# Optimization experiments

Measured on AMD Instinct MI355X. Metric: run time of the kernel, lower is better.

The kernel has to match this reference:

```python
import jax, jax.numpy as jnp
import numpy as np

S = 64            # out_size
EXPAND = 1.25
FEAT_DOWN = 8
DEG2RAD = np.pi / 180.0


def setup_inputs() -> dict:
    key = jax.random.key(0)
    k1, k2, k3 = jax.random.split(key, 3)
    B, C, Hf, Wf = 2, 64, 128, 128
    N = 256
    feat = jax.random.normal(k1, (B, C, Hf, Wf), dtype=jnp.float32)
    r = jax.random.uniform(k2, (N, 5), dtype=jnp.float32)
    # values chosen so the (buggy-but-faithful) normalized-coordinate affine
    # actually samples inside the feature map (see shape_source note)
    cx = (r[:, 0] - 0.5) * 10.0
    cy = (r[:, 1] - 0.5) * 10.0
    w = 50.0 + 350.0 * r[:, 2]
    h = 50.0 + 350.0 * r[:, 3]
    deg = (r[:, 4] - 0.5) * 180.0
    obb = jnp.stack([cx, cy, w, h, deg], axis=1)
    bix = jax.random.randint(k3, (N,), 0, B)
    return {"feat": feat, "obb": obb, "bix": bix}


def _grids(obb):
    """Replicates obb_to_affine + F.affine_grid(align_corners=False).
    Returns normalized grid coords gx, gy of shape (N, S, S)."""
    scale = 1.0 / FEAT_DOWN
    cx = obb[:, 0] * scale
    cy = obb[:, 1] * scale
    ws = obb[:, 2] * scale * EXPAND
    hs = obb[:, 3] * scale * EXPAND
    th = obb[:, 4] * DEG2RAD
    c = jnp.cos(th)
    s_ = jnp.sin(th)
    sx = ws / S
    sy = hs / S
    # faithful to source: M = [[c*sx, -sin*sy, cx], [expand*sx, c*sy, cy]]
    m00 = c * sx
    m01 = -s_ * sy
    m02 = cx
    m10 = EXPAND * sx   # source uses `s` = expand here, NOT sin(theta)
    m11 = c * sy
    m12 = cy
    # affine_grid base coords (align_corners=False): (2k+1)/S - 1
    base = (2.0 * jnp.arange(S, dtype=obb.dtype) + 1.0) / S - 1.0
    x = base[None, None, :]   # output column -> x
    y = base[None, :, None]   # output row    -> y
    gx = m00[:, None, None] * x + m01[:, None, None] * y + m02[:, None, None]
    gy = m10[:, None, None] * x + m11[:, None, None] * y + m12[:, None, None]
    return gx, gy


def _rotated_roi_pool(feat, obb, bix):
    B, C, Hf, Wf = feat.shape
    gx, gy = _grids(obb)                       # (N,S,S)
    # grid_sample unnormalize (align_corners=False)
    ix = ((gx + 1.0) * Wf - 1.0) * 0.5
    iy = ((gy + 1.0) * Hf - 1.0) * 0.5
    x0f = jnp.floor(ix)
    y0f = jnp.floor(iy)
    wx1 = ix - x0f
    wy1 = iy - y0f
    x0 = x0f.astype(jnp.int32)
    y0 = y0f.astype(jnp.int32)
    b = bix[:, None, None].astype(jnp.int32)   # (N,1,1)

    def corner(yi, xi):
        valid = (xi >= 0) & (xi < Wf) & (yi >= 0) & (yi < Hf)
        yc = jnp.clip(yi, 0, Hf - 1)
        xc = jnp.clip(xi, 0, Wf - 1)
        v = feat[b, :, yc, xc]                 # (N,S,S,C) gather
        return v * valid[..., None].astype(feat.dtype)

    out = (corner(y0, x0)         * ((1.0 - wy1) * (1.0 - wx1))[..., None]
         + corner(y0, x0 + 1)     * ((1.0 - wy1) * wx1)[..., None]
         + corner(y0 + 1, x0)     * (wy1 * (1.0 - wx1))[..., None]
         + corner(y0 + 1, x0 + 1) * (wy1 * wx1)[..., None])
    return jnp.transpose(out, (0, 3, 1, 2))    # (N,C,S,S)


def reference(feat, obb, bix):
    return _rotated_roi_pool(feat, obb, bix)
```

## Files before the change

kernel.cpp:

```cpp
#include <hip/hip_runtime.h>
#include <math.h>

#define S 64
#define NC 64
#define HF 128
#define WF 128
#define HW (HF * WF)
#define SS (S * S)
#define EXPANDF 1.25f
#define FEAT_DOWN_INV 0.125f
#define DEG2RADF 0.017453292519943295f

typedef float vfloat4 __attribute__((ext_vector_type(4)));

__device__ __forceinline__ unsigned int f32_to_bf16_rne(float v) {
    unsigned int u = __float_as_uint(v);
    return (u + 0x7FFFu + ((u >> 16) & 1u)) >> 16;
}
__device__ __forceinline__ float bf16_bits_to_f32(unsigned int h) {
    return __uint_as_float(h << 16);
}

__global__ __launch_bounds__(256) void nchw_to_nhwc_bf16_kernel(
    const float*    __restrict__ feat,
    unsigned short* __restrict__ featT)
{
    __shared__ float lds[64 * 65];
    const int bh  = blockIdx.x;
    const int b   = bh >> 7;
    const int h   = bh & (HF - 1);
    const int w0  = blockIdx.y << 6;
    const int tid = threadIdx.x;
    const int t4  = tid >> 6;
    const int t64 = tid & 63;

#pragma unroll
    for (int k = 0; k < 16; ++k) {
        const int c = (k << 2) + t4;
        lds[t64 * 65 + c] = feat[(((size_t)b * NC + c) * HF + h) * WF + w0 + t64];
    }
    __syncthreads();
#pragma unroll
    for (int k = 0; k < 16; ++k) {
        const int w = (k << 2) + t4;
        featT[(((size_t)b * HF + h) * WF + w0 + w) * NC + t64] =
            (unsigned short)f32_to_bf16_rne(lds[w * 65 + t64]);
    }
}

__global__ __launch_bounds__(256) void RotatedROIPool_kernel(
    const unsigned short* __restrict__ featT,
    const float*          __restrict__ obb,
    const int*            __restrict__ bix,
    float*                __restrict__ out,
    int nwg_per_xcd)
{
    __shared__ float lds[64 * 65];

    const int bid = blockIdx.x;
    const int wg  = (bid & 7) * nwg_per_xcd + (bid >> 3);
    const int n   = wg >> 6;
    const int i   = wg & 63;

    const int tid  = threadIdx.x;
    const int wv   = tid >> 6;
    const int lane = tid & 63;
    const int s    = lane >> 3;
    const int c8   = lane & 7;

    const float o0 = obb[n * 5 + 0];
    const float o1 = obb[n * 5 + 1];
    const float o2 = obb[n * 5 + 2];
    const float o3 = obb[n * 5 + 3];
    const float o4 = obb[n * 5 + 4];

    const float cx  = o0 * FEAT_DOWN_INV;
    const float cy  = o1 * FEAT_DOWN_INV;
    const float wsc = o2 * FEAT_DOWN_INV * EXPANDF;
    const float hsc = o3 * FEAT_DOWN_INV * EXPANDF;
    const float th  = o4 * DEG2RADF;

    float sth, cth;
    sincosf(th, &sth, &cth);

    const float sx  = wsc * (1.0f / (float)S);
    const float sy  = hsc * (1.0f / (float)S);
    const float m00 = cth * sx;
    const float m01 = -sth * sy;
    const float m10 = EXPANDF * sx;
    const float m11 = cth * sy;

    const float yg = (2.0f * (float)i + 1.0f) * (1.0f / (float)S) - 1.0f;
    const float hx = m01 * yg + cx;
    const float hy = m11 * yg + cy;

    const int b = bix[n];
    const unsigned char* __restrict__ pb =
        (const unsigned char*)featT + (size_t)b * ((size_t)HW * NC * 2);

#pragma unroll
    for (int sg = 0; sg < 2; ++sg) {
        const int j = (wv << 4) + (sg << 3) + s;

        const float xg = (2.0f * (float)j + 1.0f) * (1.0f / (float)S) - 1.0f;
        const float gx = m00 * xg + hx;
        const float gy = m10 * xg + hy;

        const float ix = ((gx + 1.0f) * (float)WF - 1.0f) * 0.5f;
        const float iy = ((gy + 1.0f) * (float)HF - 1.0f) * 0.5f;

        const float x0f = floorf(ix);
        const float y0f = floorf(iy);
        const float wx1 = ix - x0f;
        const float wy1 = iy - y0f;
        const float wx0 = 1.0f - wx1;
        const float wy0 = 1.0f - wy1;

        const int x0 = (int)x0f;
        const int y0 = (int)y0f;
        const int x1 = x0 + 1;
        const int y1 = y0 + 1;

        const float vx0 = (x0 >= 0 && x0 < WF) ? 1.0f : 0.0f;
        const float vx1 = (x1 >= 0 && x1 < WF) ? 1.0f : 0.0f;
        const float vy0 = (y0 >= 0 && y0 < HF) ? 1.0f : 0.0f;
        const float vy1 = (y1 >= 0 && y1 < HF) ? 1.0f : 0.0f;

        const float w00 = wy0 * wx0 * vy0 * vx0;
        const float w01 = wy0 * wx1 * vy0 * vx1;
        const float w10 = wy1 * wx0 * vy1 * vx0;
        const float w11 = wy1 * wx1 * vy1 * vx1;

        const int x0c = min(max(x0, 0), WF - 1);
        const int x1c = min(max(x1, 0), WF - 1);
        const int y0c = min(max(y0, 0), HF - 1);
        const int y1c = min(max(y1, 0), HF - 1);

        const uint4 a00 = *((const uint4*)(pb + ((size_t)(y0c * WF + x0c) << 7)) + c8);
        const uint4 a01 = *((const uint4*)(pb + ((size_t)(y0c * WF + x1c) << 7)) + c8);
        const uint4 a10 = *((const uint4*)(pb + ((size_t)(y1c * WF + x0c) << 7)) + c8);
        const uint4 a11 = *((const uint4*)(pb + ((size_t)(y1c * WF + x1c) << 7)) + c8);

        const unsigned int* u00 = (const unsigned int*)&a00;
        const unsigned int* u01 = (const unsigned int*)&a01;
        const unsigned int* u10 = (const unsigned int*)&a10;
        const unsigned int* u11 = (const unsigned int*)&a11;

        float* L = lds + j * 65 + (c8 << 3);
#pragma unroll
        for (int m = 0; m < 4; ++m) {
            const float f00l = bf16_bits_to_f32(u00[m] & 0xFFFFu);
            const float f01l = bf16_bits_to_f32(u01[m] & 0xFFFFu);
            const float f10l = bf16_bits_to_f32(u10[m] & 0xFFFFu);
            const float f11l = bf16_bits_to_f32(u11[m] & 0xFFFFu);
            const float f00h = bf16_bits_to_f32(u00[m] >> 16);
            const float f01h = bf16_bits_to_f32(u01[m] >> 16);
            const float f10h = bf16_bits_to_f32(u10[m] >> 16);
            const float f11h = bf16_bits_to_f32(u11[m] >> 16);
            L[2 * m + 0] = w00 * f00l + w01 * f01l + w10 * f10l + w11 * f11l;
            L[2 * m + 1] = w00 * f00h + w01 * f01h + w10 * f10h + w11 * f11h;
        }
    }

    __syncthreads();

    float* __restrict__ ob = out + (size_t)n * NC * SS + (size_t)i * S;
    const int jg = tid & 15;
    const int cl = tid >> 4;
#pragma unroll
    for (int k = 0; k < 4; ++k) {
        const int c = (k << 4) + cl;
        vfloat4 t;
        t.x = lds[(jg * 4 + 0) * 65 + c];
        t.y = lds[(jg * 4 + 1) * 65 + c];
        t.z = lds[(jg * 4 + 2) * 65 + c];
        t.w = lds[(jg * 4 + 3) * 65 + c];
        __builtin_nontemporal_store(t, (vfloat4*)(ob + (size_t)c * SS + (jg << 2)));
    }
}

__global__ __launch_bounds__(256) void RotatedROIPool_nchw_kernel(
    const float* __restrict__ feat, const float* __restrict__ obb,
    const int* __restrict__ bix, float* __restrict__ out)
{
    const int tid = threadIdx.x, pid = blockIdx.x;
    const int n = pid >> 4, patch = pid & 15;
    const int pi = (patch >> 2) << 4, pj = (patch & 3) << 4;
    const int w = tid >> 6, lane = tid & 63;
    const int i = pi + ((w >> 1) << 3) + (lane >> 3);
    const int j = pj + ((w & 1) << 3) + (lane & 7);
    const int c0 = blockIdx.y * 8;

    const float cx = obb[n*5+0]*FEAT_DOWN_INV, cy = obb[n*5+1]*FEAT_DOWN_INV;
    const float wsc = obb[n*5+2]*FEAT_DOWN_INV*EXPANDF, hsc = obb[n*5+3]*FEAT_DOWN_INV*EXPANDF;
    float sth, cth; sincosf(obb[n*5+4]*DEG2RADF, &sth, &cth);
    const float sx = wsc/(float)S, sy = hsc/(float)S;
    const float m00 = cth*sx, m01 = -sth*sy, m10 = EXPANDF*sx, m11 = cth*sy;
    const float xg = (2.f*j+1.f)/(float)S - 1.f, yg = (2.f*i+1.f)/(float)S - 1.f;
    const float gx = m00*xg + m01*yg + cx, gy = m10*xg + m11*yg + cy;
    const float ix = ((gx+1.f)*WF-1.f)*.5f, iy = ((gy+1.f)*HF-1.f)*.5f;
    const float x0f = floorf(ix), y0f = floorf(iy);
    const float wx1 = ix-x0f, wy1 = iy-y0f, wx0 = 1.f-wx1, wy0 = 1.f-wy1;
    const int x0 = (int)x0f, y0 = (int)y0f, x1 = x0+1, y1 = y0+1;
    const float vx0 = (x0>=0&&x0<WF)?1.f:0.f, vx1 = (x1>=0&&x1<WF)?1.f:0.f;
    const float vy0 = (y0>=0&&y0<HF)?1.f:0.f, vy1 = (y1>=0&&y1<HF)?1.f:0.f;
    const float w00 = wy0*wx0*vy0*vx0, w01 = wy0*wx1*vy0*vx1;
    const float w10 = wy1*wx0*vy1*vx0, w11 = wy1*wx1*vy1*vx1;
    const int x0c = min(max(x0,0),WF-1), x1c = min(max(x1,0),WF-1);
    const int y0c = min(max(y0,0),HF-1), y1c = min(max(y1,0),HF-1);
    const int o00 = y0c*WF+x0c, o01 = y0c*WF+x1c, o10 = y1c*WF+x0c, o11 = y1c*WF+x1c;
    const float* p = feat + (size_t)bix[n]*NC*HW + (size_t)c0*HW;
    float* op = out + (size_t)n*NC*SS + (size_t)c0*SS + (size_t)i*S + j;
#pragma unroll
    for (int g = 0; g < 2; ++g) {
        float v00[4], v01[4], v10[4], v11[4];
        const float* pc = p + (size_t)g*4*HW;
#pragma unroll
        for (int c = 0; c < 4; ++c) { v00[c]=pc[o00]; v01[c]=pc[o01]; v10[c]=pc[o10]; v11[c]=pc[o11]; pc += HW; }
        float* oc = op + (size_t)g*4*SS;
#pragma unroll
        for (int c = 0; c < 4; ++c) { *oc = w00*v00[c]+w01*v01[c]+w10*v10[c]+w11*v11[c]; oc += SS; }
    }
}

extern "C" void kernel_launch(void* const* d_in, const int* in_sizes, int n_in,
                              void* d_out, int out_size, void* d_ws, size_t ws_size,
                              hipStream_t stream) {
    const float* feat = (const float*)d_in[0];
    const float* obb  = (const float*)d_in[1];
    const int*   bx   = (const int*)d_in[2];
    float* out = (float*)d_out;

    const int N = in_sizes[1] / 5;
    const int B = in_sizes[0] / (NC * HW);
    const size_t tbytes = (size_t)B * NC * HW * sizeof(unsigned short);

    if (ws_size >= tbytes) {
        unsigned short* featT = (unsigned short*)d_ws;
        dim3 tg(B * HF, WF / 64, 1);
        nchw_to_nhwc_bf16_kernel<<<tg, 256, 0, stream>>>(feat, featT);

        const int nwg = N * S;
        RotatedROIPool_kernel<<<nwg, 256, 0, stream>>>(featT, obb, bx, out, nwg / 8);
    } else {
        dim3 grid(N * 16, NC / 8, 1);
        RotatedROIPool_nchw_kernel<<<grid, 256, 0, stream>>>(feat, obb, bx, out);
    }
}
```

Baseline: 59.02 us.

## Issue all gathers up front and split LDS transpose into two halves

All eight corner gathers for both column halves are issued before any compute, so more memory requests are in flight. The LDS transpose and output store are then done in two halves of 32 columns with separate buffers, so the first half's stores can begin while the second half is still being combined. This raises register pressure from holding eight uint4 values, and adds a second barrier.

```diff
diff --git a/kernel.cpp b/kernel.cpp
--- a/kernel.cpp
+++ b/kernel.cpp
@@ -55,7 +55,7 @@
     float*                __restrict__ out,
     int nwg_per_xcd)
 {
-    __shared__ float lds[64 * 65];
+    __shared__ float lds[2][32 * 65];
 
     const int bid = blockIdx.x;
     const int wg  = (bid & 7) * nwg_per_xcd + (bid >> 3);
@@ -67,6 +67,7 @@
     const int lane = tid & 63;
     const int s    = lane >> 3;
     const int c8   = lane & 7;
+    const int jj   = (wv << 3) + s;
 
     const float o0 = obb[n * 5 + 0];
     const float o1 = obb[n * 5 + 1];
@@ -98,9 +99,11 @@
     const unsigned char* __restrict__ pb =
         (const unsigned char*)featT + (size_t)b * ((size_t)HW * NC * 2);
 
-#pragma unroll
-    for (int sg = 0; sg < 2; ++sg) {
-        const int j = (wv << 4) + (sg << 3) + s;
+    uint4 a00[2], a01[2], a10[2], a11[2];
+    float w00[2], w01[2], w10[2], w11[2];
+#pragma unroll
+    for (int h = 0; h < 2; ++h) {
+        const int j = (h << 5) + jj;
 
         const float xg = (2.0f * (float)j + 1.0f) * (1.0f / (float)S) - 1.0f;
         const float gx = m00 * xg + hx;
@@ -126,27 +129,33 @@
         const float vy0 = (y0 >= 0 && y0 < HF) ? 1.0f : 0.0f;
         const float vy1 = (y1 >= 0 && y1 < HF) ? 1.0f : 0.0f;
 
-        const float w00 = wy0 * wx0 * vy0 * vx0;
-        const float w01 = wy0 * wx1 * vy0 * vx1;
-        const float w10 = wy1 * wx0 * vy1 * vx0;
-        const float w11 = wy1 * wx1 * vy1 * vx1;
+        w00[h] = wy0 * wx0 * vy0 * vx0;
+        w01[h] = wy0 * wx1 * vy0 * vx1;
+        w10[h] = wy1 * wx0 * vy1 * vx0;
+        w11[h] = wy1 * wx1 * vy1 * vx1;
 
         const int x0c = min(max(x0, 0), WF - 1);
         const int x1c = min(max(x1, 0), WF - 1);
         const int y0c = min(max(y0, 0), HF - 1);
         const int y1c = min(max(y1, 0), HF - 1);
 
-        const uint4 a00 = *((const uint4*)(pb + ((size_t)(y0c * WF + x0c) << 7)) + c8);
-        const uint4 a01 = *((const uint4*)(pb + ((size_t)(y0c * WF + x1c) << 7)) + c8);
-        const uint4 a10 = *((const uint4*)(pb + ((size_t)(y1c * WF + x0c) << 7)) + c8);
-        const uint4 a11 = *((const uint4*)(pb + ((size_t)(y1c * WF + x1c) << 7)) + c8);
-
-        const unsigned int* u00 = (const unsigned int*)&a00;
-        const unsigned int* u01 = (const unsigned int*)&a01;
-        const unsigned int* u10 = (const unsigned int*)&a10;
-        const unsigned int* u11 = (const unsigned int*)&a11;
-
-        float* L = lds + j * 65 + (c8 << 3);
+        a00[h] = *((const uint4*)(pb + ((size_t)(y0c * WF + x0c) << 7)) + c8);
+        a01[h] = *((const uint4*)(pb + ((size_t)(y0c * WF + x1c) << 7)) + c8);
+        a10[h] = *((const uint4*)(pb + ((size_t)(y1c * WF + x0c) << 7)) + c8);
+        a11[h] = *((const uint4*)(pb + ((size_t)(y1c * WF + x1c) << 7)) + c8);
+    }
+
+    const int jg = tid & 7;
+    const int cl = tid >> 3;
+    float* __restrict__ ob = out + (size_t)n * NC * SS + (size_t)i * S;
+
+#pragma unroll
+    for (int h = 0; h < 2; ++h) {
+        const unsigned int* u00 = (const unsigned int*)&a00[h];
+        const unsigned int* u01 = (const unsigned int*)&a01[h];
+        const unsigned int* u10 = (const unsigned int*)&a10[h];
+        const unsigned int* u11 = (const unsigned int*)&a11[h];
+        float* L = lds[h] + jj * 65 + (c8 << 3);
 #pragma unroll
         for (int m = 0; m < 4; ++m) {
             const float f00l = bf16_bits_to_f32(u00[m] & 0xFFFFu);
@@ -157,25 +166,22 @@
             const float f01h = bf16_bits_to_f32(u01[m] >> 16);
             const float f10h = bf16_bits_to_f32(u10[m] >> 16);
             const float f11h = bf16_bits_to_f32(u11[m] >> 16);
-            L[2 * m + 0] = w00 * f00l + w01 * f01l + w10 * f10l + w11 * f11l;
-            L[2 * m + 1] = w00 * f00h + w01 * f01h + w10 * f10h + w11 * f11h;
+            L[2 * m + 0] = w00[h] * f00l + w01[h] * f01l + w10[h] * f10l + w11[h] * f11l;
+            L[2 * m + 1] = w00[h] * f00h + w01[h] * f01h + w10[h] * f10h + w11[h] * f11h;
         }
-    }
-
-    __syncthreads();
-
-    float* __restrict__ ob = out + (size_t)n * NC * SS + (size_t)i * S;
-    const int jg = tid & 15;
-    const int cl = tid >> 4;
-#pragma unroll
-    for (int k = 0; k < 4; ++k) {
-        const int c = (k << 4) + cl;
-        vfloat4 t;
-        t.x = lds[(jg * 4 + 0) * 65 + c];
-        t.y = lds[(jg * 4 + 1) * 65 + c];
-        t.z = lds[(jg * 4 + 2) * 65 + c];
-        t.w = lds[(jg * 4 + 3) * 65 + c];
-        __builtin_nontemporal_store(t, (vfloat4*)(ob + (size_t)c * SS + (jg << 2)));
+
+        __syncthreads();
+
+#pragma unroll
+        for (int k = 0; k < 2; ++k) {
+            const int c = (k << 5) + cl;
+            vfloat4 t;
+            t.x = lds[h][(jg * 4 + 0) * 65 + c];
+            t.y = lds[h][(jg * 4 + 1) * 65 + c];
+            t.z = lds[h][(jg * 4 + 2) * 65 + c];
+            t.w = lds[h][(jg * 4 + 3) * 65 + c];
+            __builtin_nontemporal_store(t, (vfloat4*)(ob + (size_t)c * SS + (h << 5) + (jg << 2)));
+        }
     }
 }
 
```

New measurement: 60.30 us. +2.2%, slower.
